# Kernel tuning notes

Measured on AMD Instinct MI355X. Metric: run time of the kernel, lower is better.

The kernel has to match this reference:

```python
import jax, jax.numpy as jnp
import numpy as np

# Model dims (Mamba2-2.7B-like)
B_SZ = 1; SEQ = 2048; HID = 2048
INTER = 4096; N_STATE = 128; N_GROUPS = 1; NH = 64; HD = 64
K_CONV = 4; CHUNK = 256
GN = N_GROUPS * N_STATE            # 128
CONV_DIM = INTER + 2 * GN          # 4352
D_IN = 2 * INTER + 2 * GN + NH     # 8512
EPS = 1e-5


def setup_inputs() -> dict:
    key = jax.random.key(0)
    ks = jax.random.split(key, 8)
    return {
        "hidden_states": jax.random.normal(ks[0], (B_SZ, SEQ, HID), jnp.float32),
        "W_in": jax.random.normal(ks[1], (HID, D_IN), jnp.float32) * 0.02,
        "conv_w": jax.random.normal(ks[2], (CONV_DIM, K_CONV), jnp.float32) * 0.2,
        "conv_b": jax.random.normal(ks[3], (CONV_DIM,), jnp.float32) * 0.1,
        "dt_bias": jax.random.uniform(ks[4], (NH,), jnp.float32, -4.0, 0.0),
        "A": -jnp.exp(jax.random.uniform(ks[5], (NH,), jnp.float32, -1.0, 1.0)),
        "D": jnp.ones((NH,), jnp.float32),
        "norm_weight": jnp.ones((INTER,), jnp.float32),
        "W_out": jax.random.normal(ks[6], (INTER, HID), jnp.float32) * 0.02,
    }


def reference(hidden_states, W_in, conv_w, conv_b, dt_bias, A, D, norm_weight, W_out):
    b, S, _ = hidden_states.shape
    # in_proj and split: gate [inter], x/B/C [conv_dim], dt [num_heads]
    proj = hidden_states @ W_in
    gate, xBC, dt = jnp.split(proj, [INTER, INTER + CONV_DIM], axis=-1)
    dt = jax.nn.softplus(dt + dt_bias)  # [b,S,NH]

    # causal depthwise conv1d + SiLU (kernel K, left-padded)
    xp = jnp.pad(xBC, ((0, 0), (K_CONV - 1, 0), (0, 0)))
    conv = conv_b
    for k in range(K_CONV):  # tiny fixed loop over kernel taps
        conv = conv + conv_w[:, k] * xp[:, k:k + S, :]
    xBC = jax.nn.silu(conv)

    x, Bm, Cm = jnp.split(xBC, [INTER, INTER + GN], axis=-1)
    L = CHUNK; nc = S // L
    x_c = x.reshape(b, nc, L, NH, HD)
    rep = NH // N_GROUPS
    B_c = jnp.repeat(Bm.reshape(b, nc, L, N_GROUPS, N_STATE), rep, axis=3)  # bclhn
    C_c = jnp.repeat(Cm.reshape(b, nc, L, N_GROUPS, N_STATE), rep, axis=3)
    dt_c = dt.reshape(b, nc, L, NH)

    dA = dt_c * A                      # [b,c,l,h]  (A < 0)
    cA = jnp.cumsum(dA, axis=2)        # within-chunk cumulative log-decay
    cAt = jnp.transpose(cA, (0, 1, 3, 2))  # [b,c,h,l]

    # intra-chunk: causal decay matrix, (C B^T) masked, weighted by dt
    diff = cAt[..., :, None] - cAt[..., None, :]          # [b,c,h,l,s]
    tril = jnp.tril(jnp.ones((L, L), bool))
    Lmat = jnp.exp(jnp.where(tril, diff, -jnp.inf))
    CB = jnp.einsum('bclhn,bcshn->bchls', C_c, B_c)
    M = CB * Lmat * jnp.transpose(dt_c, (0, 1, 3, 2))[:, :, :, None, :]
    Y_intra = jnp.einsum('bchls,bcshp->bclhp', M, x_c)

    # per-chunk end state contributions
    decay_states = jnp.exp(cA[:, :, -1:, :] - cA)          # [b,c,l,h]
    states = jnp.einsum('bclh,bclhn,bclhp->bchpn', decay_states * dt_c, B_c, x_c)
    chunk_decay = jnp.exp(cA[:, :, -1, :])                 # [b,c,h]

    def step(carry, inp):
        d, st = inp
        new = carry * d[..., None, None] + st
        return new, carry  # emit state entering the chunk

    _, prev = jax.lax.scan(step, jnp.zeros((b, NH, HD, N_STATE), states.dtype),
                           (jnp.moveaxis(chunk_decay, 1, 0), jnp.moveaxis(states, 1, 0)))
    prev = jnp.moveaxis(prev, 0, 1)                        # [b,c,h,p,n]

    Y_inter = jnp.einsum('bclhn,bclh,bchpn->bclhp', C_c, jnp.exp(cA), prev)
    Y = Y_intra + Y_inter + x_c * D[:, None]               # skip D*x per head

    y = Y.reshape(b, S, INTER)
    # gated RMSNorm in fp32
    z = y.astype(jnp.float32) * jax.nn.silu(gate.astype(jnp.float32))
    var = jnp.mean(z * z, axis=-1, keepdims=True)
    z = z * jax.lax.rsqrt(var + EPS) * norm_weight
    return z @ W_out
```

## Files before the change

kernel.cpp:

```cpp
#include <hip/hip_runtime.h>

typedef __bf16 bf16_t;
typedef bf16_t bf16x8 __attribute__((ext_vector_type(8)));
typedef float f32x4 __attribute__((ext_vector_type(4)));
typedef unsigned short u16;
typedef u16 u16x8 __attribute__((ext_vector_type(8)));
typedef u16 u16x4 __attribute__((ext_vector_type(4)));

#define SEQ   2048
#define HID   2048
#define INTER 4096
#define NH    64
#define HD    64
#define CONVD 4352
#define DIN   8512
#define LDP   8576L
#define CHNK  256
#define NC    8

__device__ __forceinline__ u16 f2bf(float f) {
  union { float f; unsigned u; } a; a.f = f;
  return (u16)((a.u + 0x7fffu + ((a.u >> 16) & 1u)) >> 16);
}
__device__ __forceinline__ float bf2f(u16 u) {
  union { unsigned u; float f; } a; a.u = ((unsigned)u) << 16;
  return a.f;
}

__device__ __forceinline__ void gl2lds16(const void* g, void* l) {
  auto gp = reinterpret_cast<__attribute__((address_space(1))) void*>(
      (unsigned long long)g);
  auto lp = reinterpret_cast<__attribute__((address_space(3))) void*>(
      (unsigned)(unsigned long long)l);
  __builtin_amdgcn_global_load_lds(gp, lp, 16, 0, 0);
}

__global__ __launch_bounds__(256) void cvt_bf16(const float* __restrict__ s,
                                                u16* __restrict__ d, int n4) {
  int i = blockIdx.x * 256 + threadIdx.x;
  if (i < n4) {
    f32x4 v = ((const f32x4*)s)[i];
    u16x4 r;
#pragma unroll
    for (int k = 0; k < 4; ++k) r[k] = f2bf(v[k]);
    ((u16x4*)d)[i] = r;
  }
}

__global__ void transpose_bf16(const float* __restrict__ src, u16* __restrict__ dst,
                               int R, int Cc) {
  __shared__ float t[32][33];
  int n0 = blockIdx.x * 32, k0 = blockIdx.y * 32;
  int tx = threadIdx.x, ty = threadIdx.y;
  for (int i = ty; i < 32; i += 8) {
    int n = n0 + tx;
    t[i][tx] = (n < Cc) ? src[(long)(k0 + i) * Cc + n] : 0.f;
  }
  __syncthreads();
  for (int i = ty; i < 32; i += 8)
    dst[(long)(n0 + i) * R + k0 + tx] = f2bf(t[tx][i]);
}

__global__ __launch_bounds__(256, 2) void gemm_bt(const u16* __restrict__ A,
                                                  const u16* __restrict__ Bt,
                                                  float* __restrict__ C,
                                                  int N, int lda, int Klen,
                                                  long zstride) {
  __shared__ __align__(16) u16 As[128 * 64];
  __shared__ __align__(16) u16 Bs[128 * 64];
  const int kz = blockIdx.z;
  A  += (long)kz * Klen;
  Bt += (long)kz * Klen;
  C  += (long)kz * zstride;
  const int nb = gridDim.x * gridDim.y;
  const int id = blockIdx.x + gridDim.x * blockIdx.y;
  const int s = (id & 7) * (nb >> 3) + (id >> 3);
  const long bm = s & 15;
  const long bn = s >> 4;

  const int tid = threadIdx.x;
  const int lane = tid & 63;
  const int w = tid >> 6;
  const int wm = w >> 1, wn = w & 1;

  f32x4 acc[4][4];
#pragma unroll
  for (int i = 0; i < 4; ++i)
#pragma unroll
    for (int j = 0; j < 4; ++j) acc[i][j] = (f32x4){0.f, 0.f, 0.f, 0.f};

  const int srr = lane >> 3;
  const int sc8 = ((lane & 7) ^ srr) * 8;
  const u16* Agw = A + (bm * 128 + w * 8 + srr) * (long)lda + sc8;
  const u16* Bgw = Bt + (bn * 128 + w * 8 + srr) * (long)lda + sc8;
  u16* ldA = As + w * 512 + lane * 8;
  u16* ldB = Bs + w * 512 + lane * 8;
  const int fr = lane & 15, q = lane >> 4;
  const int fx = (fr & 7) << 3;

  for (int k0 = 0; k0 < Klen; k0 += 64) {
    __syncthreads();
#pragma unroll
    for (int t = 0; t < 4; ++t) {
      gl2lds16(Agw + k0 + (long)t * 32 * lda, ldA + t * 2048);
      gl2lds16(Bgw + k0 + (long)t * 32 * lda, ldB + t * 2048);
    }
    __builtin_amdgcn_s_waitcnt(0);
    __syncthreads();
#pragma unroll
    for (int ks = 0; ks < 2; ++ks) {
      bf16x8 af[4], bfv[4];
#pragma unroll
      for (int i = 0; i < 4; ++i)
        af[i] = *(const bf16x8*)(As + ((wm * 64 + i * 16 + fr) << 6) +
                                 ((((ks << 2) + q) << 3) ^ fx));
#pragma unroll
      for (int j = 0; j < 4; ++j)
        bfv[j] = *(const bf16x8*)(Bs + ((wn * 64 + j * 16 + fr) << 6) +
                                  ((((ks << 2) + q) << 3) ^ fx));
#pragma unroll
      for (int i = 0; i < 4; ++i)
#pragma unroll
        for (int j = 0; j < 4; ++j)
          acc[i][j] = __builtin_amdgcn_mfma_f32_16x16x32_bf16(af[i], bfv[j], acc[i][j], 0, 0, 0);
    }
  }
  const int cr = (lane >> 4) * 4;
  const int cc = lane & 15;
#pragma unroll
  for (int i = 0; i < 4; ++i)
#pragma unroll
    for (int j = 0; j < 4; ++j) {
      long r = bm * 128 + wm * 64 + i * 16 + cr;
      long cidx = bn * 128 + wn * 64 + j * 16 + cc;
      float* cp = C + r * (long)N + cidx;
#pragma unroll
      for (int t = 0; t < 4; ++t) cp[(long)t * N] = acc[i][j][t];
    }
}

__global__ __launch_bounds__(256) void add2_kernel(const float* __restrict__ a,
                                                   const float* __restrict__ b,
                                                   float* __restrict__ o) {
  int i = blockIdx.x * 256 + threadIdx.x;
  ((f32x4*)o)[i] = ((const f32x4*)a)[i] + ((const f32x4*)b)[i];
}

__global__ __launch_bounds__(256) void conv_silu_t(const float* __restrict__ proj,
                                                   const float* __restrict__ cw,
                                                   const float* __restrict__ cb,
                                                   u16* __restrict__ xbf,
                                                   u16* __restrict__ xT) {
  __shared__ float ld[35][33];
  __shared__ u16 tt[32][34];
  const int c0 = blockIdx.x * 32, t0 = blockIdx.y * 32;
  const int tx = threadIdx.x & 31, ty = threadIdx.x >> 5;
  for (int i = ty; i < 35; i += 8) {
    int t = t0 - 3 + i;
    ld[i][tx] = (t >= 0) ? proj[(long)t * LDP + INTER + c0 + tx] : 0.f;
  }
  const int c = c0 + tx;
  const float w0 = cw[c * 4 + 0], w1 = cw[c * 4 + 1], w2 = cw[c * 4 + 2],
              w3 = cw[c * 4 + 3], bias = cb[c];
  __syncthreads();
  for (int i = ty; i < 32; i += 8) {
    float a = bias + w0 * ld[i][tx] + w1 * ld[i + 1][tx] + w2 * ld[i + 2][tx] +
              w3 * ld[i + 3][tx];
    u16 v = f2bf(a / (1.f + __expf(-a)));
    xbf[(long)(t0 + i) * CONVD + c] = v;
    tt[i][tx] = v;
  }
  __syncthreads();
  if (c0 < 4224) {
    for (int i = ty; i < 32; i += 8)
      xT[(long)(c0 + i) * 2048 + t0 + tx] = tt[tx][i];
  }
}

__global__ __launch_bounds__(256) void dt_cumsum(const float* __restrict__ proj,
                                                 const float* __restrict__ dtb,
                                                 const float* __restrict__ A,
                                                 float* __restrict__ dt2,
                                                 float* __restrict__ cA2) {
  __shared__ float sc[256];
  int c = blockIdx.x, h = blockIdx.y, l = threadIdx.x;
  float v = proj[(long)(c * 256 + l) * LDP + 8448 + h] + dtb[h];
  float sp = (v > 20.f) ? v : log1pf(__expf(v));
  dt2[h * 2048 + c * 256 + l] = sp;
  sc[l] = sp * A[h];
  __syncthreads();
  for (int off = 1; off < 256; off <<= 1) {
    float t = (l >= off) ? sc[l - off] : 0.f;
    __syncthreads();
    sc[l] += t;
    __syncthreads();
  }
  cA2[h * 2048 + c * 256 + l] = sc[l];
}

__global__ __launch_bounds__(256, 2) void cb_gemm(const u16* __restrict__ xbf,
                                                  float* __restrict__ CB) {
  __shared__ __align__(16) u16 As[128 * 32];
  __shared__ __align__(16) u16 Bs[128 * 32];
  const int tid = threadIdx.x;
  const int lane = tid & 63;
  const int w = tid >> 6;
  const int wm = w >> 1, wn = w & 1;
  const int bm = blockIdx.y, bn = blockIdx.x, c = blockIdx.z;

  f32x4 acc[4][4];
#pragma unroll
  for (int i = 0; i < 4; ++i)
#pragma unroll
    for (int j = 0; j < 4; ++j) acc[i][j] = (f32x4){0.f, 0.f, 0.f, 0.f};

  const int sr = w * 32 + (lane >> 2);
  const int sc = ((lane & 3) ^ ((lane >> 2) & 3)) * 8;
  const u16* Ag = xbf + (long)(c * 256 + bm * 128) * CONVD + 4224;
  const u16* Bg = xbf + (long)(c * 256 + bn * 128) * CONVD + 4096;
  u16* lA0 = As + w * 1024 + lane * 8;
  u16* lA1 = As + w * 1024 + 512 + lane * 8;
  u16* lB0 = Bs + w * 1024 + lane * 8;
  u16* lB1 = Bs + w * 1024 + 512 + lane * 8;
  const int fr = lane & 15, q = lane >> 4;
  const int pc = ((q ^ (fr & 3)) << 3);

  for (int k0 = 0; k0 < 128; k0 += 32) {
    __syncthreads();
    const u16* a0 = Ag + (long)sr * CONVD + k0 + sc;
    const u16* b0 = Bg + (long)sr * CONVD + k0 + sc;
    gl2lds16(a0, lA0);
    gl2lds16(a0 + 16L * CONVD, lA1);
    gl2lds16(b0, lB0);
    gl2lds16(b0 + 16L * CONVD, lB1);
    __builtin_amdgcn_s_waitcnt(0);
    __syncthreads();
    bf16x8 af[4], bfv[4];
#pragma unroll
    for (int i = 0; i < 4; ++i)
      af[i] = *(const bf16x8*)(As + ((wm * 64 + i * 16 + fr) << 5) + pc);
#pragma unroll
    for (int j = 0; j < 4; ++j)
      bfv[j] = *(const bf16x8*)(Bs + ((wn * 64 + j * 16 + fr) << 5) + pc);
#pragma unroll
    for (int i = 0; i < 4; ++i)
#pragma unroll
      for (int j = 0; j < 4; ++j)
        acc[i][j] = __builtin_amdgcn_mfma_f32_16x16x32_bf16(af[i], bfv[j], acc[i][j], 0, 0, 0);
  }
  const int cr = (lane >> 4) * 4;
  const int cc = lane & 15;
  float* Cc = CB + (long)c * 65536;
#pragma unroll
  for (int i = 0; i < 4; ++i)
#pragma unroll
    for (int j = 0; j < 4; ++j) {
      int r = bm * 128 + wm * 64 + i * 16 + cr;
      int cidx = bn * 128 + wn * 64 + j * 16 + cc;
      float* cp = Cc + (long)r * 256 + cidx;
#pragma unroll
      for (int t = 0; t < 4; ++t) cp[t * 256] = acc[i][j][t];
    }
}

#define LDM 72
__global__ __launch_bounds__(256) void states_kernel(const u16* __restrict__ xT,
                                                     const float* __restrict__ dt2,
                                                     const float* __restrict__ cA2,
                                                     float* __restrict__ stT) {
  __shared__ __align__(16) u16 Ms[128 * LDM];
  __shared__ __align__(16) u16 Xs[64 * LDM];
  __shared__ float wl[256];
  const int c = blockIdx.x, h = blockIdx.y;
  const int tid = threadIdx.x;
  const int lane = tid & 63, w = tid >> 6;
  const int fr = lane & 15, q = lane >> 4;
  {
    float calast = cA2[h * 2048 + c * 256 + 255];
    float ca = cA2[h * 2048 + c * 256 + tid];
    wl[tid] = __expf(calast - ca) * dt2[h * 2048 + c * 256 + tid];
  }
  f32x4 acc[2][4];
#pragma unroll
  for (int i = 0; i < 2; ++i)
#pragma unroll
    for (int j = 0; j < 4; ++j) acc[i][j] = (f32x4){0.f, 0.f, 0.f, 0.f};

  const int lc8 = (tid & 7) * 8;
  const int rn = tid >> 3;
  __syncthreads();

  for (int kt = 0; kt < 4; ++kt) {
    __syncthreads();
#pragma unroll
    for (int r = 0; r < 4; ++r) {
      int n = rn + 32 * r;
      u16x8 raw = *(const u16x8*)(xT + (long)(4096 + n) * 2048 + c * 256 + kt * 64 + lc8);
      union { u16 u[8]; bf16x8 v; } pk;
#pragma unroll
      for (int u = 0; u < 8; ++u)
        pk.u[u] = f2bf(bf2f(raw[u]) * wl[kt * 64 + lc8 + u]);
      *(bf16x8*)(Ms + n * LDM + lc8) = pk.v;
    }
#pragma unroll
    for (int r = 0; r < 2; ++r) {
      int p = rn + 32 * r;
      *(bf16x8*)(Xs + p * LDM + lc8) =
          *(const bf16x8*)(xT + (long)(h * 64 + p) * 2048 + c * 256 + kt * 64 + lc8);
    }
    __syncthreads();
#pragma unroll
    for (int ks = 0; ks < 64; ks += 32) {
      bf16x8 af[2], xf[4];
#pragma unroll
      for (int i = 0; i < 2; ++i)
        af[i] = *(const bf16x8*)(Ms + (w * 32 + i * 16 + fr) * LDM + ks + q * 8);
#pragma unroll
      for (int j = 0; j < 4; ++j)
        xf[j] = *(const bf16x8*)(Xs + (j * 16 + fr) * LDM + ks + q * 8);
#pragma unroll
      for (int i = 0; i < 2; ++i)
#pragma unroll
        for (int j = 0; j < 4; ++j)
          acc[i][j] = __builtin_amdgcn_mfma_f32_16x16x32_bf16(af[i], xf[j], acc[i][j], 0, 0, 0);
    }
  }
  const int cr = (lane >> 4) * 4;
  const int cc = lane & 15;
  float* outp = stT + (long)(c * 64 + h) * 8192;
#pragma unroll
  for (int i = 0; i < 2; ++i)
#pragma unroll
    for (int j = 0; j < 4; ++j) {
      int n = w * 32 + i * 16 + cr;
      int p = j * 16 + cc;
#pragma unroll
      for (int t = 0; t < 4; ++t) outp[(n + t) * 64 + p] = acc[i][j][t];
    }
}

__global__ __launch_bounds__(256) void scan_kernel(const float* __restrict__ stT,
                                                   const float* __restrict__ cA2,
                                                   float* __restrict__ prevT) {
  int id = blockIdx.x * 256 + threadIdx.x;
  int h = id >> 13;
  float acc = 0.f;
#pragma unroll
  for (int c = 0; c < NC; ++c) {
    prevT[(long)c * 524288 + id] = acc;
    float cd = __expf(cA2[h * 2048 + c * 256 + 255]);
    acc = acc * cd + stT[(long)c * 524288 + id];
  }
}

__global__ __launch_bounds__(256) void ssm_y_kernel(const u16* __restrict__ xbf,
                                                    const u16* __restrict__ xT,
                                                    const float* __restrict__ dt2,
                                                    const float* __restrict__ cA2,
                                                    const float* __restrict__ CB,
                                                    const float* __restrict__ prevT,
                                                    const float* __restrict__ Dp,
                                                    u16* __restrict__ Y) {
  __shared__ __align__(16) u16 Ms[256 * LDM];
  __shared__ __align__(16) u16 Xt[64 * LDM];
  __shared__ float cas[256];
  __shared__ float dts[256];
  const int c = blockIdx.x, h = blockIdx.y;
  const int tid = threadIdx.x;
  const int lane = tid & 63;
  const int w = tid >> 6;
  const int fr = lane & 15, q = lane >> 4;

  cas[tid] = cA2[h * 2048 + c * 256 + tid];
  dts[tid] = dt2[h * 2048 + c * 256 + tid];

  f32x4 acc[4][4];
#pragma unroll
  for (int i = 0; i < 4; ++i)
#pragma unroll
    for (int j = 0; j < 4; ++j) acc[i][j] = (f32x4){0.f, 0.f, 0.f, 0.f};

  const int sg = (tid & 7) * 8;
  const int lb = tid >> 3;
  const int xp = tid & 63;
  const int xq = tid >> 6;

  __syncthreads();

  for (int kt = 0; kt < 6; ++kt) {
    __syncthreads();
    if (kt < 4) {
      const int s0 = kt * 64;
      f32x4 e0 = *(const f32x4*)&cas[s0 + sg];
      f32x4 e1 = *(const f32x4*)&cas[s0 + sg + 4];
      f32x4 d0 = *(const f32x4*)&dts[s0 + sg];
      f32x4 d1 = *(const f32x4*)&dts[s0 + sg + 4];
#pragma unroll
      for (int k = 0; k < 8; ++k) {
        const int l = lb + 32 * k;
        const float cal = cas[l];
        const float* cb = CB + (long)c * 65536 + (long)l * 256 + s0 + sg;
        f32x4 c0 = *(const f32x4*)cb;
        f32x4 c1 = *(const f32x4*)(cb + 4);
        union { u16 u[8]; bf16x8 v; } pk;
#pragma unroll
        for (int u = 0; u < 8; ++u) {
          int s = s0 + sg + u;
          float cv = (u < 4) ? c0[u] : c1[u - 4];
          float cs = (u < 4) ? e0[u] : e1[u - 4];
          float dv = (u < 4) ? d0[u] : d1[u - 4];
          float m = (s <= l) ? cv * __expf(cal - cs) * dv : 0.f;
          pk.u[u] = f2bf(m);
        }
        *(bf16x8*)(Ms + l * LDM + sg) = pk.v;
      }
#pragma unroll
      for (int r = 0; r < 2; ++r) {
        int p = (tid >> 3) + 32 * r;
        *(bf16x8*)(Xt + p * LDM + sg) =
            *(const bf16x8*)(xT + (long)(h * 64 + p) * 2048 + c * 256 + s0 + sg);
      }
    } else {
      const int n0 = (kt - 4) * 64;
#pragma unroll
      for (int k = 0; k < 8; ++k) {
        const int l = lb + 32 * k;
        const float ea = __expf(cas[l]);
        u16x8 raw = *(const u16x8*)(xbf + (long)(c * 256 + l) * CONVD + 4224 + n0 + sg);
        union { u16 u[8]; bf16x8 v; } pk;
#pragma unroll
        for (int u = 0; u < 8; ++u) pk.u[u] = f2bf(ea * bf2f(raw[u]));
        *(bf16x8*)(Ms + l * LDM + sg) = pk.v;
      }
      const float* pT = prevT + (long)(c * 64 + h) * 8192;
#pragma unroll
      for (int half = 0; half < 2; ++half) {
        const int nb2 = xq * 16 + half * 8;
        union { u16 u[8]; bf16x8 v; } pk;
#pragma unroll
        for (int u = 0; u < 8; ++u) pk.u[u] = f2bf(pT[(n0 + nb2 + u) * 64 + xp]);
        *(bf16x8*)(Xt + xp * LDM + nb2) = pk.v;
      }
    }
    __syncthreads();
#pragma unroll
    for (int ks = 0; ks < 64; ks += 32) {
      bf16x8 af[4], bfv[4];
#pragma unroll
      for (int i = 0; i < 4; ++i)
        af[i] = *(const bf16x8*)(Ms + (w * 64 + i * 16 + fr) * LDM + ks + q * 8);
#pragma unroll
      for (int j = 0; j < 4; ++j)
        bfv[j] = *(const bf16x8*)(Xt + (j * 16 + fr) * LDM + ks + q * 8);
#pragma unroll
      for (int i = 0; i < 4; ++i)
#pragma unroll
        for (int j = 0; j < 4; ++j)
          acc[i][j] = __builtin_amdgcn_mfma_f32_16x16x32_bf16(af[i], bfv[j], acc[i][j], 0, 0, 0);
    }
  }

  const int cr = (lane >> 4) * 4;
  const int cc = lane & 15;
  const float dh = Dp[h];
#pragma unroll
  for (int i = 0; i < 4; ++i)
#pragma unroll
    for (int j = 0; j < 4; ++j) {
      const int p = j * 16 + cc;
#pragma unroll
      for (int t = 0; t < 4; ++t) {
        const int row = w * 64 + i * 16 + cr + t;
        const float xv = bf2f(xbf[(long)(c * 256 + row) * CONVD + h * 64 + p]);
        Y[(long)(c * 256 + row) * 4096 + h * 64 + p] = f2bf(acc[i][j][t] + dh * xv);
      }
    }
}

__global__ __launch_bounds__(256) void rmsnorm_kernel(const u16* __restrict__ Y,
                                                      const float* __restrict__ proj,
                                                      const float* __restrict__ nw,
                                                      u16* __restrict__ zbf) {
  __shared__ float red[256];
  int t = blockIdx.x, tid = threadIdx.x;
  const u16* y = Y + (long)t * 4096;
  const float* g = proj + (long)t * LDP;
  float zv[16];
  float s = 0.f;
#pragma unroll
  for (int k = 0; k < 16; ++k) {
    int i = tid + k * 256;
    float gv = g[i];
    float z = bf2f(y[i]) * (gv / (1.f + __expf(-gv)));
    zv[k] = z;
    s += z * z;
  }
  red[tid] = s;
  __syncthreads();
  if (tid < 128) red[tid] += red[tid + 128];
  __syncthreads();
  if (tid < 64) {
    float v = red[tid] + red[tid + 64];
    v += __shfl_down(v, 32);
    v += __shfl_down(v, 16);
    v += __shfl_down(v, 8);
    v += __shfl_down(v, 4);
    v += __shfl_down(v, 2);
    v += __shfl_down(v, 1);
    if (tid == 0) red[0] = v;
  }
  __syncthreads();
  float scale = rsqrtf(red[0] * (1.f / 4096.f) + 1e-5f);
#pragma unroll
  for (int k = 0; k < 16; ++k) {
    int i = tid + k * 256;
    zbf[(long)t * 4096 + i] = f2bf(zv[k] * scale * nw[i]);
  }
}

extern "C" void kernel_launch(void* const* d_in, const int* in_sizes, int n_in,
                              void* d_out, int out_size, void* d_ws, size_t ws_size,
                              hipStream_t stream) {
  const float* hidden = (const float*)d_in[0];
  const float* Win    = (const float*)d_in[1];
  const float* convw  = (const float*)d_in[2];
  const float* convb  = (const float*)d_in[3];
  const float* dtb    = (const float*)d_in[4];
  const float* Ap     = (const float*)d_in[5];
  const float* Dp     = (const float*)d_in[6];
  const float* nw     = (const float*)d_in[7];
  const float* Wout   = (const float*)d_in[8];
  float* out = (float*)d_out;
  char* ws = (char*)d_ws;

  u16*   hb    = (u16*)(ws + 0);
  u16*   WinT  = (u16*)(ws + 8388608L);
  float* proj  = (float*)(ws + 43515904L);
  u16*   WoutT = (u16*)(ws + 113770496L);
  u16*   xbf   = (u16*)(ws + 130547712L);
  u16*   xT    = (u16*)(ws + 148373504L);
  float* dt2   = (float*)(ws + 165675008L);
  float* cA2   = (float*)(ws + 166199296L);
  float* CBv   = (float*)(ws + 166723584L);
  float* stT   = (float*)(ws + 168820736L);
  float* prevT = (float*)(ws + 185597952L);
  u16*   zbf   = (u16*)(ws + 202375168L);
  u16*   Y     = (u16*)(ws + 0);
  float* Cp    = (float*)(ws + 43515904L);

  cvt_bf16<<<4096, 256, 0, stream>>>(hidden, hb, 1048576);
  transpose_bf16<<<dim3(268, 64), dim3(32, 8), 0, stream>>>(Win, WinT, 2048, 8512);
  transpose_bf16<<<dim3(64, 128), dim3(32, 8), 0, stream>>>(Wout, WoutT, 4096, 2048);
  gemm_bt<<<dim3(67, 16, 1), 256, 0, stream>>>(hb, WinT, proj, 8576, 2048, 2048, 0L);
  conv_silu_t<<<dim3(136, 64), 256, 0, stream>>>(proj, convw, convb, xbf, xT);
  dt_cumsum<<<dim3(8, 64), 256, 0, stream>>>(proj, dtb, Ap, dt2, cA2);
  cb_gemm<<<dim3(2, 2, 8), 256, 0, stream>>>(xbf, CBv);
  states_kernel<<<dim3(8, 64), 256, 0, stream>>>(xT, dt2, cA2, stT);
  scan_kernel<<<2048, 256, 0, stream>>>(stT, cA2, prevT);
  ssm_y_kernel<<<dim3(8, 64), 256, 0, stream>>>(xbf, xT, dt2, cA2, CBv, prevT, Dp, Y);
  rmsnorm_kernel<<<2048, 256, 0, stream>>>(Y, proj, nw, zbf);
  gemm_bt<<<dim3(16, 16, 2), 256, 0, stream>>>(zbf, WoutT, Cp, 2048, 4096, 2048, 4194304L);
  add2_kernel<<<4096, 256, 0, stream>>>(Cp, Cp + 4194304, out);
}
```

Measured before the change: 415.9 us.

## Add 256x256-tile pipelined GEMM kernel for in and out projections

Adds a new 512-thread GEMM with 256x256 output tiles, a 4-slot LDS ring buffer with swizzled direct global-to-LDS loads, interleaved quarter-tile MFMA phases, and s_setprio around the MFMA bursts. It replaces the 128x128 gemm_bt for the bulk of in_proj; the 384-column remainder stays on the old kernel. out_proj becomes a 4-way split-K, followed by a 4-input reduction kernel. The aim is more operand reuse per LDS load and better latency hiding, at the cost of a 256-block grid that may underfill the CUs and extra partial-sum traffic from split-K.

```diff
diff --git a/kernel.cpp b/kernel.cpp
--- a/kernel.cpp
+++ b/kernel.cpp
@@ -139,11 +139,175 @@
     }
 }
 
-__global__ __launch_bounds__(256) void add2_kernel(const float* __restrict__ a,
-                                                   const float* __restrict__ b,
+#define MFMA16(ACC, AF, BF)                                                    \
+  _Pragma("unroll") for (int i_ = 0; i_ < 4; ++i_)                             \
+  _Pragma("unroll") for (int j_ = 0; j_ < 2; ++j_) {                           \
+    ACC[i_][j_] = __builtin_amdgcn_mfma_f32_16x16x32_bf16(                     \
+        AF[i_][0], BF[j_][0], ACC[i_][j_], 0, 0, 0);                           \
+    ACC[i_][j_] = __builtin_amdgcn_mfma_f32_16x16x32_bf16(                     \
+        AF[i_][1], BF[j_][1], ACC[i_][j_], 0, 0, 0);                           \
+  }
+
+#define LDAF(DST, SLOT)                                                        \
+  _Pragma("unroll") for (int i_ = 0; i_ < 4; ++i_) {                           \
+    const u16* p_ = Abuf[SLOT] + ((wm * 64 + i_ * 16 + fr) << 6);              \
+    DST[i_][0] = *(const bf16x8*)(p_ + ke0);                                   \
+    DST[i_][1] = *(const bf16x8*)(p_ + ke1);                                   \
+  }
+
+#define LDBF(DST, SLOT)                                                        \
+  _Pragma("unroll") for (int j_ = 0; j_ < 2; ++j_) {                           \
+    const u16* p_ = Bbuf[SLOT] + ((wn * 32 + j_ * 16 + fr) << 6);              \
+    DST[j_][0] = *(const bf16x8*)(p_ + ke0);                                   \
+    DST[j_][1] = *(const bf16x8*)(p_ + ke1);                                   \
+  }
+
+#define STAGE(G, HO, KO, SLOT, BUF)                                            \
+  {                                                                            \
+    const u16* g_ = (G) + (HO) + (KO);                                         \
+    gl2lds16(g_ + off1, BUF[SLOT] + lo1);                                      \
+    gl2lds16(g_ + off2, BUF[SLOT] + lo2);                                      \
+  }
+
+__global__ __launch_bounds__(512, 2) void gemm256(const u16* __restrict__ A,
+                                                  const u16* __restrict__ Bt,
+                                                  float* __restrict__ C,
+                                                  int N, int lda, int Klen,
+                                                  long zstride) {
+  __shared__ __align__(16) u16 Abuf[4][128 * 64];
+  __shared__ __align__(16) u16 Bbuf[4][128 * 64];
+
+  const int kz = blockIdx.z;
+  A  += (long)kz * Klen;
+  Bt += (long)kz * Klen;
+  C  += (long)kz * zstride;
+
+  const int nb = gridDim.x * gridDim.y;
+  const int id = blockIdx.x + gridDim.x * blockIdx.y;
+  const int s = (id & 7) * (nb >> 3) + (id >> 3);
+  const long bm = s & 7;
+  const long bn = s >> 3;
+
+  const int tid = threadIdx.x;
+  const int lane = tid & 63;
+  const int w = tid >> 6;
+  const int wm = w >> 2;
+  const int wn = w & 3;
+  const int fr = lane & 15, q = lane >> 4;
+  const int ke0 = (q ^ (fr & 7)) << 3;
+  const int ke1 = ((4 + q) ^ (fr & 7)) << 3;
+
+  const int sr1 = (w << 4) + (lane >> 3);
+  const int sr2 = sr1 + 8;
+  const int kcp = lane & 7;
+  const long off1 = (long)sr1 * lda + ((kcp ^ (sr1 & 7)) << 3);
+  const long off2 = (long)sr2 * lda + ((kcp ^ (sr2 & 7)) << 3);
+  const int lo1 = (w << 10) + (lane << 3);
+  const int lo2 = lo1 + 512;
+  const long h128 = 128L * lda;
+
+  const u16* gA = A + bm * 256 * lda;
+  const u16* gB = Bt + bn * 256 * lda;
+
+  f32x4 acc00[4][2], acc01[4][2], acc10[4][2], acc11[4][2];
+#pragma unroll
+  for (int i = 0; i < 4; ++i)
+#pragma unroll
+    for (int j = 0; j < 2; ++j) {
+      acc00[i][j] = (f32x4){0.f, 0.f, 0.f, 0.f};
+      acc01[i][j] = (f32x4){0.f, 0.f, 0.f, 0.f};
+      acc10[i][j] = (f32x4){0.f, 0.f, 0.f, 0.f};
+      acc11[i][j] = (f32x4){0.f, 0.f, 0.f, 0.f};
+    }
+
+  const int NT = Klen >> 6;
+
+  STAGE(gA, 0L, 0L, 0, Abuf);
+  STAGE(gB, 0L, 0L, 0, Bbuf);
+  STAGE(gB, h128, 0L, 1, Bbuf);
+  STAGE(gA, h128, 0L, 1, Abuf);
+  STAGE(gA, 0L, 64L, 2, Abuf);
+  STAGE(gB, 0L, 64L, 2, Bbuf);
+  asm volatile("s_waitcnt vmcnt(6)" ::: "memory");
+  __builtin_amdgcn_s_barrier();
+
+  for (int T = 0; T < NT; ++T) {
+    const int t2 = (T << 1) & 3;
+    const int t2p1 = (t2 + 1) & 3;
+    const int t2p3 = (t2 + 3) & 3;
+    const long kT1 = (long)(T + 1) << 6;
+    const long kT2 = (long)(T + 2) << 6;
+    const bool g1 = (T + 1 < NT), g2 = (T + 2 < NT);
+    bf16x8 a0[4][2], a1[4][2], b0[2][2], b1[2][2];
+
+    LDAF(a0, t2);
+    LDBF(b0, t2);
+    if (g1) STAGE(gB, h128, kT1, t2p3, Bbuf);
+    __builtin_amdgcn_s_barrier();
+    __builtin_amdgcn_s_setprio(1);
+    MFMA16(acc00, a0, b0);
+    __builtin_amdgcn_s_setprio(0);
+    __builtin_amdgcn_s_barrier();
+
+    LDBF(b1, t2p1);
+    if (g1) STAGE(gA, h128, kT1, t2p3, Abuf);
+    __builtin_amdgcn_s_barrier();
+    __builtin_amdgcn_s_setprio(1);
+    MFMA16(acc01, a0, b1);
+    __builtin_amdgcn_s_setprio(0);
+    asm volatile("s_waitcnt vmcnt(6)" ::: "memory");
+    __builtin_amdgcn_s_barrier();
+
+    LDAF(a1, t2p1);
+    if (g2) STAGE(gA, 0L, kT2, t2, Abuf);
+    __builtin_amdgcn_s_barrier();
+    __builtin_amdgcn_s_setprio(1);
+    MFMA16(acc10, a1, b0);
+    __builtin_amdgcn_s_setprio(0);
+    __builtin_amdgcn_s_barrier();
+
+    if (g2) STAGE(gB, 0L, kT2, t2, Bbuf);
+    __builtin_amdgcn_s_barrier();
+    __builtin_amdgcn_s_setprio(1);
+    MFMA16(acc11, a1, b1);
+    __builtin_amdgcn_s_setprio(0);
+    if (T == NT - 2)
+      asm volatile("s_waitcnt vmcnt(0)" ::: "memory");
+    else
+      asm volatile("s_waitcnt vmcnt(6)" ::: "memory");
+    __builtin_amdgcn_s_barrier();
+  }
+
+  const int cr = (lane >> 4) << 2;
+  const int cc = lane & 15;
+  const long r0 = bm * 256 + wm * 64 + cr;
+  const long c0 = bn * 256 + wn * 32 + cc;
+#define CWRITE(ACC, QA, QB)                                                    \
+  _Pragma("unroll") for (int i_ = 0; i_ < 4; ++i_)                             \
+  _Pragma("unroll") for (int j_ = 0; j_ < 2; ++j_) {                           \
+    long r_ = r0 + (QA)*128 + i_ * 16;                                         \
+    long c_ = c0 + (QB)*128 + j_ * 16;                                         \
+    if (c_ < N) {                                                              \
+      float* cp_ = C + r_ * (long)N + c_;                                      \
+      _Pragma("unroll") for (int t_ = 0; t_ < 4; ++t_)                         \
+          cp_[(long)t_ * N] = ACC[i_][j_][t_];                                 \
+    }                                                                          \
+  }
+  CWRITE(acc00, 0, 0)
+  CWRITE(acc01, 0, 1)
+  CWRITE(acc10, 1, 0)
+  CWRITE(acc11, 1, 1)
+#undef CWRITE
+}
+
+__global__ __launch_bounds__(256) void add4_kernel(const float* __restrict__ a,
                                                    float* __restrict__ o) {
   int i = blockIdx.x * 256 + threadIdx.x;
-  ((f32x4*)o)[i] = ((const f32x4*)a)[i] + ((const f32x4*)b)[i];
+  f32x4 r = ((const f32x4*)a)[i];
+  r += ((const f32x4*)(a + 4194304L))[i];
+  r += ((const f32x4*)(a + 8388608L))[i];
+  r += ((const f32x4*)(a + 12582912L))[i];
+  ((f32x4*)o)[i] = r;
 }
 
 __global__ __launch_bounds__(256) void conv_silu_t(const float* __restrict__ proj,
@@ -551,7 +715,9 @@
   cvt_bf16<<<4096, 256, 0, stream>>>(hidden, hb, 1048576);
   transpose_bf16<<<dim3(268, 64), dim3(32, 8), 0, stream>>>(Win, WinT, 2048, 8512);
   transpose_bf16<<<dim3(64, 128), dim3(32, 8), 0, stream>>>(Wout, WoutT, 4096, 2048);
-  gemm_bt<<<dim3(67, 16, 1), 256, 0, stream>>>(hb, WinT, proj, 8576, 2048, 2048, 0L);
+  gemm256<<<dim3(32, 8, 1), 512, 0, stream>>>(hb, WinT, proj, 8576, 2048, 2048, 0L);
+  gemm_bt<<<dim3(3, 16, 1), 256, 0, stream>>>(hb, WinT + 8192L * 2048, proj + 8192,
+                                              8576, 2048, 2048, 0L);
   conv_silu_t<<<dim3(136, 64), 256, 0, stream>>>(proj, convw, convb, xbf, xT);
   dt_cumsum<<<dim3(8, 64), 256, 0, stream>>>(proj, dtb, Ap, dt2, cA2);
   cb_gemm<<<dim3(2, 2, 8), 256, 0, stream>>>(xbf, CBv);
@@ -559,6 +725,6 @@
   scan_kernel<<<2048, 256, 0, stream>>>(stT, cA2, prevT);
   ssm_y_kernel<<<dim3(8, 64), 256, 0, stream>>>(xbf, xT, dt2, cA2, CBv, prevT, Dp, Y);
   rmsnorm_kernel<<<2048, 256, 0, stream>>>(Y, proj, nw, zbf);
-  gemm_bt<<<dim3(16, 16, 2), 256, 0, stream>>>(zbf, WoutT, Cp, 2048, 4096, 2048, 4194304L);
-  add2_kernel<<<4096, 256, 0, stream>>>(Cp, Cp + 4194304, out);
-}
+  gemm256<<<dim3(8, 8, 4), 512, 0, stream>>>(zbf, WoutT, Cp, 2048, 4096, 1024, 4194304L);
+  add4_kernel<<<4096, 256, 0, stream>>>(Cp, out);
+}
```

Result: no change. 418.5 us (+0.6%).

## Software-pipeline GEMM with 4-stage LDS ring and async prefetch

Applied to the files above, without the earlier changes.

Rewrites the bf16 GEMM main loop to use K-tiles of 32 held in a 4-deep LDS ring buffer. Tiles are prefetched two steps ahead with global_load_lds and gated by vmcnt waits, so global loads overlap MFMA work instead of each tile being loaded and fully drained before compute. It also adds explicit ds_read_b128 inline asm, a new XOR swizzle, and raised wave priority around the MFMAs. The cost is more LDS per block, which may limit occupancy, and hand-tuned waitcnt logic that depends on exact instruction counts.

```diff
diff --git a/kernel.cpp b/kernel.cpp
--- a/kernel.cpp
+++ b/kernel.cpp
@@ -35,6 +35,12 @@
   __builtin_amdgcn_global_load_lds(gp, lp, 16, 0, 0);
 }
 
+__device__ __forceinline__ bf16x8 ds128(unsigned addr) {
+  bf16x8 r;
+  asm volatile("ds_read_b128 %0, %1" : "=v"(r) : "v"(addr));
+  return r;
+}
+
 __global__ __launch_bounds__(256) void cvt_bf16(const float* __restrict__ s,
                                                 u16* __restrict__ d, int n4) {
   int i = blockIdx.x * 256 + threadIdx.x;
@@ -61,17 +67,19 @@
     dst[(long)(n0 + i) * R + k0 + tx] = f2bf(t[tx][i]);
 }
 
-__global__ __launch_bounds__(256, 2) void gemm_bt(const u16* __restrict__ A,
+__global__ __launch_bounds__(256, 2) void gemm_hp(const u16* __restrict__ A,
                                                   const u16* __restrict__ Bt,
                                                   float* __restrict__ C,
                                                   int N, int lda, int Klen,
                                                   long zstride) {
-  __shared__ __align__(16) u16 As[128 * 64];
-  __shared__ __align__(16) u16 Bs[128 * 64];
+  __shared__ __align__(16) u16 Abuf[4][128 * 32];
+  __shared__ __align__(16) u16 Bbuf[4][128 * 32];
+
   const int kz = blockIdx.z;
   A  += (long)kz * Klen;
   Bt += (long)kz * Klen;
   C  += (long)kz * zstride;
+
   const int nb = gridDim.x * gridDim.y;
   const int id = blockIdx.x + gridDim.x * blockIdx.y;
   const int s = (id & 7) * (nb >> 3) + (id >> 3);
@@ -82,6 +90,16 @@
   const int lane = tid & 63;
   const int w = tid >> 6;
   const int wm = w >> 1, wn = w & 1;
+  const int fr = lane & 15, q = lane >> 4;
+
+  const int r1 = tid >> 2;
+  const int kc = tid & 3;
+  const long soff1 = (long)r1 * lda + ((kc ^ (r1 & 3)) << 3);
+  const long soff2 = (long)(r1 + 64) * lda + ((kc ^ (r1 & 3)) << 3);
+  const int ld1 = tid << 3;
+  const int ld2 = ld1 + 2048;
+  const u16* gA = A + bm * 128 * (long)lda;
+  const u16* gB = Bt + bn * 128 * (long)lda;
 
   f32x4 acc[4][4];
 #pragma unroll
@@ -89,42 +107,55 @@
 #pragma unroll
     for (int j = 0; j < 4; ++j) acc[i][j] = (f32x4){0.f, 0.f, 0.f, 0.f};
 
-  const int srr = lane >> 3;
-  const int sc8 = ((lane & 7) ^ srr) * 8;
-  const u16* Agw = A + (bm * 128 + w * 8 + srr) * (long)lda + sc8;
-  const u16* Bgw = Bt + (bn * 128 + w * 8 + srr) * (long)lda + sc8;
-  u16* ldA = As + w * 512 + lane * 8;
-  u16* ldB = Bs + w * 512 + lane * 8;
-  const int fr = lane & 15, q = lane >> 4;
-  const int fx = (fr & 7) << 3;
-
-  for (int k0 = 0; k0 < Klen; k0 += 64) {
-    __syncthreads();
-#pragma unroll
-    for (int t = 0; t < 4; ++t) {
-      gl2lds16(Agw + k0 + (long)t * 32 * lda, ldA + t * 2048);
-      gl2lds16(Bgw + k0 + (long)t * 32 * lda, ldB + t * 2048);
-    }
-    __builtin_amdgcn_s_waitcnt(0);
-    __syncthreads();
-#pragma unroll
-    for (int ks = 0; ks < 2; ++ks) {
-      bf16x8 af[4], bfv[4];
-#pragma unroll
-      for (int i = 0; i < 4; ++i)
-        af[i] = *(const bf16x8*)(As + ((wm * 64 + i * 16 + fr) << 6) +
-                                 ((((ks << 2) + q) << 3) ^ fx));
+  const unsigned abase = (unsigned)(unsigned long long)(&Abuf[0][0]);
+  const unsigned bbase = (unsigned)(unsigned long long)(&Bbuf[0][0]);
+  const int fq = (q ^ (fr & 3)) << 4;
+  const unsigned aro = (unsigned)((wm * 64 + fr) * 64 + fq);
+  const unsigned bro = (unsigned)((wn * 64 + fr) * 64 + fq);
+
+#define STG(kt)                                                                \
+  {                                                                            \
+    const long ko_ = (long)(kt) << 5;                                          \
+    u16* la_ = &Abuf[(kt) & 3][0];                                             \
+    u16* lb_ = &Bbuf[(kt) & 3][0];                                             \
+    gl2lds16(gA + ko_ + soff1, la_ + ld1);                                     \
+    gl2lds16(gA + ko_ + soff2, la_ + ld2);                                     \
+    gl2lds16(gB + ko_ + soff1, lb_ + ld1);                                     \
+    gl2lds16(gB + ko_ + soff2, lb_ + ld2);                                     \
+  }
+
+  const int NT = Klen >> 5;
+
+  STG(0);
+  STG(1);
+  asm volatile("s_waitcnt vmcnt(4)" ::: "memory");
+  __builtin_amdgcn_s_barrier();
+
+  for (int T = 0; T < NT; ++T) {
+    if (T + 2 < NT) STG(T + 2);
+    const unsigned sb = (unsigned)((T & 3) << 13);
+    bf16x8 af[4], bfv[4];
+#pragma unroll
+    for (int i = 0; i < 4; ++i) af[i] = ds128(abase + sb + aro + i * 1024u);
+#pragma unroll
+    for (int j = 0; j < 4; ++j) bfv[j] = ds128(bbase + sb + bro + j * 1024u);
+    asm volatile("s_waitcnt lgkmcnt(0)" ::: "memory");
+    __builtin_amdgcn_sched_barrier(0);
+    __builtin_amdgcn_s_setprio(1);
+#pragma unroll
+    for (int i = 0; i < 4; ++i)
 #pragma unroll
       for (int j = 0; j < 4; ++j)
-        bfv[j] = *(const bf16x8*)(Bs + ((wn * 64 + j * 16 + fr) << 6) +
-                                  ((((ks << 2) + q) << 3) ^ fx));
-#pragma unroll
-      for (int i = 0; i < 4; ++i)
-#pragma unroll
-        for (int j = 0; j < 4; ++j)
-          acc[i][j] = __builtin_amdgcn_mfma_f32_16x16x32_bf16(af[i], bfv[j], acc[i][j], 0, 0, 0);
-    }
-  }
+        acc[i][j] = __builtin_amdgcn_mfma_f32_16x16x32_bf16(af[i], bfv[j], acc[i][j], 0, 0, 0);
+    __builtin_amdgcn_s_setprio(0);
+    if (T + 2 < NT)
+      asm volatile("s_waitcnt vmcnt(4)" ::: "memory");
+    else
+      asm volatile("s_waitcnt vmcnt(0)" ::: "memory");
+    __builtin_amdgcn_s_barrier();
+  }
+#undef STG
+
   const int cr = (lane >> 4) * 4;
   const int cc = lane & 15;
 #pragma unroll
@@ -551,7 +582,7 @@
   cvt_bf16<<<4096, 256, 0, stream>>>(hidden, hb, 1048576);
   transpose_bf16<<<dim3(268, 64), dim3(32, 8), 0, stream>>>(Win, WinT, 2048, 8512);
   transpose_bf16<<<dim3(64, 128), dim3(32, 8), 0, stream>>>(Wout, WoutT, 4096, 2048);
-  gemm_bt<<<dim3(67, 16, 1), 256, 0, stream>>>(hb, WinT, proj, 8576, 2048, 2048, 0L);
+  gemm_hp<<<dim3(67, 16, 1), 256, 0, stream>>>(hb, WinT, proj, 8576, 2048, 2048, 0L);
   conv_silu_t<<<dim3(136, 64), 256, 0, stream>>>(proj, convw, convb, xbf, xT);
   dt_cumsum<<<dim3(8, 64), 256, 0, stream>>>(proj, dtb, Ap, dt2, cA2);
   cb_gemm<<<dim3(2, 2, 8), 256, 0, stream>>>(xbf, CBv);
@@ -559,6 +590,6 @@
   scan_kernel<<<2048, 256, 0, stream>>>(stT, cA2, prevT);
   ssm_y_kernel<<<dim3(8, 64), 256, 0, stream>>>(xbf, xT, dt2, cA2, CBv, prevT, Dp, Y);
   rmsnorm_kernel<<<2048, 256, 0, stream>>>(Y, proj, nw, zbf);
-  gemm_bt<<<dim3(16, 16, 2), 256, 0, stream>>>(zbf, WoutT, Cp, 2048, 4096, 2048, 4194304L);
-  add2_kernel<<<4096, 256, 0, stream>>>(Cp, Cp + 4194304, out);
-}
+  gemm_hp<<<dim3(16, 16, 2), 256, 0, stream>>>(zbf, WoutT, Cp, 2048, 4096, 2048, 4194304L);
+  add2_kernel<<<4096, 256, 0, stream>>>(Cp, Cp + 4194304L, out);
+}
```

Result: no change. 417.8 us (+0.5%).
